# Optimization experiments

Hardware: AMD Instinct MI355X
Metric: run time of the kernel (lower is better)

Reference implementation:

```python
import jax, jax.numpy as jnp
import numpy as np

N = 50000
E = 800000
NODE_IN = 16
EDGE_IN = 8
HID = 128
OUT = 128
HEADS = 4
HC = HID // HEADS          # per-head channels = 32
EH = HID // 2              # edge hidden = 64
EPS = 1e-5
NEG_SLOPE = 0.2            # PyG GATConv leaky_relu slope


def setup_inputs() -> dict:
    key = jax.random.key(0)
    ks = list(jax.random.split(key, 16))
    it = iter(ks)
    nx = lambda: next(it)
    s = 0.05
    p = {}
    p["x"] = jax.random.normal(nx(), (N, NODE_IN), jnp.float32)
    p["edge_index"] = jax.random.randint(nx(), (2, E), 0, N)
    p["edge_attr"] = jax.random.normal(nx(), (E, EDGE_IN), jnp.float32)
    # node_preprocess: Linear + LayerNorm
    p["np_w"] = jax.random.normal(nx(), (NODE_IN, HID), jnp.float32) * s
    p["np_b"] = jnp.zeros((HID,), jnp.float32)
    p["np_g"] = jnp.ones((HID,), jnp.float32)
    p["np_be"] = jnp.zeros((HID,), jnp.float32)
    # edge_preprocess: Linear + LayerNorm
    p["ep_w"] = jax.random.normal(nx(), (EDGE_IN, EH), jnp.float32) * s
    p["ep_b"] = jnp.zeros((EH,), jnp.float32)
    p["ep_g"] = jnp.ones((EH,), jnp.float32)
    p["ep_be"] = jnp.zeros((EH,), jnp.float32)
    # 3 stacked GATConv layers (params stacked on leading dim)
    p["gat_w"] = jax.random.normal(nx(), (3, HID, HID), jnp.float32) * s
    p["gat_as"] = jax.random.normal(nx(), (3, HEADS, HC), jnp.float32) * s
    p["gat_ad"] = jax.random.normal(nx(), (3, HEADS, HC), jnp.float32) * s
    p["gat_ew"] = jax.random.normal(nx(), (3, EH, HID), jnp.float32) * s
    p["gat_ae"] = jax.random.normal(nx(), (3, HEADS, HC), jnp.float32) * s
    p["gat_b"] = jnp.zeros((3, HID), jnp.float32)
    # BatchNorm affine params
    p["bn_g"] = jnp.ones((3, HID), jnp.float32)
    p["bn_b"] = jnp.zeros((3, HID), jnp.float32)
    # final_proj: Linear + LayerNorm
    p["fp_w"] = jax.random.normal(nx(), (HID, OUT), jnp.float32) * s
    p["fp_b"] = jnp.zeros((OUT,), jnp.float32)
    p["fp_g"] = jnp.ones((OUT,), jnp.float32)
    p["fp_be"] = jnp.zeros((OUT,), jnp.float32)
    return p


def _ln(x, g, b):
    m = x.mean(-1, keepdims=True)
    v = ((x - m) ** 2).mean(-1, keepdims=True)
    return (x - m) * jax.lax.rsqrt(v + EPS) * g + b


def _bn(x, g, b):  # training-mode batch statistics over node dim
    m = x.mean(0)
    v = ((x - m) ** 2).mean(0)
    return (x - m) * jax.lax.rsqrt(v + EPS) * g + b


def _gat(h, e, src, dst, W, a_s, a_d, We, a_e, bias):
    # h: [N, HID], e: [E2, EH], src/dst: [E2]
    xs = (h @ W).reshape(N, HEADS, HC)                       # [N,H,C]
    al_s = (xs * a_s).sum(-1)                                # [N,H]
    al_d = (xs * a_d).sum(-1)                                # [N,H]
    eh = (e @ We).reshape(-1, HEADS, HC)                     # [E2,H,C]
    alpha = al_s[src] + al_d[dst] + (eh * a_e).sum(-1)       # [E2,H]
    alpha = jnp.where(alpha >= 0, alpha, NEG_SLOPE * alpha)  # leaky relu
    # segment softmax over incoming edges of each dst node
    amax = jax.ops.segment_max(alpha, dst, num_segments=N)
    ex = jnp.exp(alpha - amax[dst])
    w = ex / jax.ops.segment_sum(ex, dst, num_segments=N)[dst]
    msg = xs[src] * w[:, :, None]                            # [E2,H,C]
    out = jax.ops.segment_sum(msg, dst, num_segments=N)      # [N,H,C]
    return out.reshape(N, HID) + bias


def reference(x, edge_index, edge_attr, np_w, np_b, np_g, np_be,
              ep_w, ep_b, ep_g, ep_be,
              gat_w, gat_as, gat_ad, gat_ew, gat_ae, gat_b,
              bn_g, bn_b, fp_w, fp_b, fp_g, fp_be):
    src, dst = edge_index[0], edge_index[1]
    h = jax.nn.relu(_ln(x @ np_w + np_b, np_g, np_be))
    e = jax.nn.relu(_ln(edge_attr @ ep_w + ep_b, ep_g, ep_be))
    # PyG GATConv default add_self_loops=True, fill_value='mean':
    # self-loop edge_attr = mean of incoming edge_attr per dst node (0 if none)
    deg = jax.ops.segment_sum(jnp.ones((E,), e.dtype), dst, num_segments=N)
    loop_e = jax.ops.segment_sum(e, dst, num_segments=N) / jnp.maximum(deg, 1.0)[:, None]
    ar = jnp.arange(N)
    src2 = jnp.concatenate([src, ar])
    dst2 = jnp.concatenate([dst, ar])
    e2 = jnp.concatenate([e, loop_e], axis=0)
    for i in range(3):
        res = h
        h = _gat(h, e2, src2, dst2, gat_w[i], gat_as[i], gat_ad[i],
                 gat_ew[i], gat_ae[i], gat_b[i])
        h = jax.nn.relu(_bn(h, bn_g[i], bn_b[i]) + res)
    return _ln(h @ fp_w + fp_b, fp_g, fp_be)
```

## Files before the change

kernel.cpp:

```cpp
#include <hip/hip_runtime.h>
#include <hip/hip_bf16.h>
#include <math.h>

#define N_NODES 50000
#define N_EDGES 800000
#define EPS 1e-5f
#define SLOPE 0.2f

typedef unsigned int u32;
typedef unsigned short u16;
typedef float floatx4 __attribute__((ext_vector_type(4)));
typedef short short8_t __attribute__((ext_vector_type(8)));

__device__ __forceinline__ float bf2f(u16 v) {
    u32 u = ((u32)v) << 16;
    return __uint_as_float(u);
}
__device__ __forceinline__ u16 f2bf(float f) {
    u32 u = __float_as_uint(f);
    u32 r = (u + 0x7fffu + ((u >> 16) & 1u)) >> 16;
    return (u16)r;
}
__device__ __forceinline__ float lo_bf(u32 v) { return __uint_as_float(v << 16); }
__device__ __forceinline__ float hi_bf(u32 v) { return __uint_as_float(v & 0xffff0000u); }
__device__ __forceinline__ float wred(float v) {
    #pragma unroll
    for (int off = 32; off > 0; off >>= 1) v += __shfl_xor(v, off, 64);
    return v;
}

__global__ void k_M(const float* __restrict__ ew, const float* __restrict__ ae,
                    float* __restrict__ M) {
    int t = threadIdx.x;
    if (t >= 768) return;
    int k = t / 12, j = t % 12;
    int l = j >> 2, h = j & 3;
    const float* ewp = ew + l * 8192 + k * 128 + h * 32;
    const float* aep = ae + l * 128 + h * 32;
    float s = 0.f;
    #pragma unroll
    for (int c = 0; c < 32; c++) s += ewp[c] * aep[c];
    M[k * 12 + j] = s;
}

__global__ void k_convW(const float* __restrict__ w, u16* __restrict__ hi,
                        u16* __restrict__ lo, int total) {
    int i = blockIdx.x * 256 + threadIdx.x;
    if (i >= total) return;
    int l = i >> 14, r = i & 16383;
    int n = r >> 7, k = r & 127;
    float f = w[(size_t)l * 16384 + k * 128 + n];
    u16 hb = f2bf(f);
    hi[i] = hb;
    lo[i] = f2bf(f - bf2f(hb));
}

__global__ __launch_bounds__(256) void k_node_pre(
        const float* __restrict__ x, const float* __restrict__ w,
        const float* __restrict__ b, const float* __restrict__ g,
        const float* __restrict__ be, float* __restrict__ h) {
    int wave = threadIdx.x >> 6, lane = threadIdx.x & 63;
    int n = blockIdx.x * 4 + wave;
    if (n >= N_NODES) return;
    const float* xr = x + (size_t)n * 16;
    float xv[16];
    #pragma unroll
    for (int k = 0; k < 16; k++) xv[k] = xr[k];
    int c0 = lane, c1 = lane + 64;
    float a0 = b[c0], a1 = b[c1];
    #pragma unroll
    for (int k = 0; k < 16; k++) {
        a0 = fmaf(xv[k], w[k * 128 + c0], a0);
        a1 = fmaf(xv[k], w[k * 128 + c1], a1);
    }
    float m = wred(a0 + a1) * (1.f / 128.f);
    float d0 = a0 - m, d1 = a1 - m;
    float v = wred(d0 * d0 + d1 * d1) * (1.f / 128.f);
    float rs = rsqrtf(v + EPS);
    float o0 = d0 * rs * g[c0] + be[c0];
    float o1 = d1 * rs * g[c1] + be[c1];
    h[(size_t)n * 128 + c0] = fmaxf(o0, 0.f);
    h[(size_t)n * 128 + c1] = fmaxf(o1, 0.f);
}

__global__ void k_deg(const int* __restrict__ dst, int* __restrict__ deg,
                      int* __restrict__ rank) {
    int e = blockIdx.x * 256 + threadIdx.x;
    if (e < N_EDGES) rank[e] = atomicAdd(&deg[dst[e]], 1);
}

__global__ void k_scan1(const int* __restrict__ deg, int* __restrict__ incl,
                        int* __restrict__ bsum) {
    __shared__ int lds[1024];
    int i = blockIdx.x * 1024 + threadIdx.x;
    int v = (i < N_NODES) ? deg[i] : 0;
    lds[threadIdx.x] = v;
    __syncthreads();
    for (int off = 1; off < 1024; off <<= 1) {
        int t = (threadIdx.x >= off) ? lds[threadIdx.x - off] : 0;
        __syncthreads();
        lds[threadIdx.x] += t;
        __syncthreads();
    }
    if (i < N_NODES) incl[i] = lds[threadIdx.x];
    if (threadIdx.x == 1023) bsum[blockIdx.x] = lds[1023];
}
__global__ void k_scan2(int* __restrict__ bsum, int nb) {
    if (threadIdx.x == 0 && blockIdx.x == 0) {
        int run = 0;
        for (int i = 0; i < nb; i++) { int t = bsum[i]; bsum[i] = run; run += t; }
    }
}
__global__ void k_scan3(const int* __restrict__ incl, const int* __restrict__ bsum,
                        int* __restrict__ rowptr) {
    int i = blockIdx.x * 1024 + threadIdx.x;
    if (i < N_NODES) rowptr[i + 1] = incl[i] + bsum[blockIdx.x];
    if (i == 0) rowptr[0] = 0;
}

__global__ void k_fill(const int* __restrict__ ei, const int* __restrict__ rowptr,
                       const int* __restrict__ rank, int2* __restrict__ csr_se) {
    int e = blockIdx.x * 256 + threadIdx.x;
    if (e >= N_EDGES) return;
    int src = ei[e], dst = ei[N_EDGES + e];
    int slot = rowptr[dst] + rank[e];
    csr_se[slot] = make_int2(src, e);
}

__global__ __launch_bounds__(256) void k_edge_c(
        const int2* __restrict__ csr_se, const float* __restrict__ ea,
        const float* __restrict__ epw, const float* __restrict__ epb,
        const float* __restrict__ epg, const float* __restrict__ epbe,
        const float* __restrict__ M, int* __restrict__ csr_src,
        float* __restrict__ csr_aE) {
    __shared__ float sW[512], sM[768], sB[64], sG[64], sBe[64];
    for (int i = threadIdx.x; i < 512; i += 256) sW[i] = epw[i];
    for (int i = threadIdx.x; i < 768; i += 256) sM[i] = M[i];
    if (threadIdx.x < 64) {
        sB[threadIdx.x] = epb[threadIdx.x];
        sG[threadIdx.x] = epg[threadIdx.x];
        sBe[threadIdx.x] = epbe[threadIdx.x];
    }
    __syncthreads();
    int t = threadIdx.x;
    int s = blockIdx.x * 128 + (t >> 1);
    if (s >= N_EDGES) return;
    int hf = t & 1, cb = hf * 32;
    int2 se = csr_se[s];
    int src = se.x, e = se.y;
    float4 x0 = *(const float4*)(ea + (size_t)e * 8);
    float4 x1 = *(const float4*)(ea + (size_t)e * 8 + 4);
    float xa[8] = {x0.x, x0.y, x0.z, x0.w, x1.x, x1.y, x1.z, x1.w};
    float v[32];
    float sum = 0.f;
    #pragma unroll
    for (int c = 0; c < 32; c++) {
        float a = sB[cb + c];
        #pragma unroll
        for (int k = 0; k < 8; k++) a = fmaf(xa[k], sW[k * 64 + cb + c], a);
        v[c] = a; sum += a;
    }
    sum += __shfl_xor(sum, 1, 64);
    float m = sum * (1.f / 64.f);
    float var = 0.f;
    #pragma unroll
    for (int c = 0; c < 32; c++) { float d = v[c] - m; var += d * d; }
    var += __shfl_xor(var, 1, 64);
    float rs = rsqrtf(var * (1.f / 64.f) + EPS);
    #pragma unroll
    for (int c = 0; c < 32; c++) {
        float o = (v[c] - m) * rs * sG[cb + c] + sBe[cb + c];
        v[c] = fmaxf(o, 0.f);
    }
    float aE[12];
    #pragma unroll
    for (int j = 0; j < 12; j++) aE[j] = 0.f;
    #pragma unroll
    for (int c = 0; c < 32; c++) {
        float vc = v[c];
        #pragma unroll
        for (int j = 0; j < 12; j++) aE[j] = fmaf(vc, sM[(cb + c) * 12 + j], aE[j]);
    }
    #pragma unroll
    for (int j = 0; j < 12; j++) aE[j] += __shfl_xor(aE[j], 1, 64);
    if (hf == 0) {
        csr_src[s] = src;
        #pragma unroll
        for (int l = 0; l < 3; l++) {
            float4 w4;
            w4.x = aE[l * 4 + 0]; w4.y = aE[l * 4 + 1];
            w4.z = aE[l * 4 + 2]; w4.w = aE[l * 4 + 3];
            *(float4*)(csr_aE + ((size_t)l * N_EDGES + s) * 4) = w4;
        }
    }
}

__global__ __launch_bounds__(256) void k_gemm_xs_mfma(
        const float* __restrict__ h, const u16* __restrict__ wt_hi,
        const u16* __restrict__ wt_lo, u16* __restrict__ xs) {
    int wave = threadIdx.x >> 6, lane = threadIdx.x & 63;
    int r0 = (blockIdx.x * 4 + wave) * 16;
    if (r0 >= N_NODES) return;
    int lrow = lane & 15, lk = lane >> 4;
    const float* ap = h + (size_t)(r0 + lrow) * 128 + lk * 8;
    const u16* bph = wt_hi + lrow * 128 + lk * 8;
    const u16* bpl = wt_lo + lrow * 128 + lk * 8;
    floatx4 acc[8];
    #pragma unroll
    for (int j = 0; j < 8; j++) acc[j] = (floatx4){0.f, 0.f, 0.f, 0.f};
    #pragma unroll
    for (int s = 0; s < 4; s++) {
        float4 v0 = *(const float4*)(ap + s * 32);
        float4 v1 = *(const float4*)(ap + s * 32 + 4);
        float av[8] = {v0.x, v0.y, v0.z, v0.w, v1.x, v1.y, v1.z, v1.w};
        short8_t ahi, alo;
        #pragma unroll
        for (int i = 0; i < 8; i++) {
            u16 hb = f2bf(av[i]);
            ahi[i] = (short)hb;
            alo[i] = (short)f2bf(av[i] - bf2f(hb));
        }
        short8_t bh[8], bl[8];
        #pragma unroll
        for (int j = 0; j < 8; j++) {
            bh[j] = *(const short8_t*)(bph + s * 32 + j * 2048);
            bl[j] = *(const short8_t*)(bpl + s * 32 + j * 2048);
        }
        #pragma unroll
        for (int j = 0; j < 8; j++)
            acc[j] = __builtin_amdgcn_mfma_f32_16x16x32_bf16(ahi, bh[j], acc[j], 0, 0, 0);
        #pragma unroll
        for (int j = 0; j < 8; j++)
            acc[j] = __builtin_amdgcn_mfma_f32_16x16x32_bf16(ahi, bl[j], acc[j], 0, 0, 0);
        #pragma unroll
        for (int j = 0; j < 8; j++)
            acc[j] = __builtin_amdgcn_mfma_f32_16x16x32_bf16(alo, bh[j], acc[j], 0, 0, 0);
    }
    u16* orow = xs + (size_t)(r0 + lk * 4) * 128 + lrow;
    #pragma unroll
    for (int j = 0; j < 8; j++) {
        #pragma unroll
        for (int reg = 0; reg < 4; reg++)
            orow[(size_t)reg * 128 + j * 16] = f2bf(acc[j][reg]);
    }
}

__global__ void k_al(const u16* __restrict__ xs, const float* __restrict__ as_,
                     const float* __restrict__ ad_, float* __restrict__ al_s,
                     float* __restrict__ al_d) {
    int t = blockIdx.x * 256 + threadIdx.x;
    if (t >= N_NODES * 4) return;
    int n = t >> 2, hh = t & 3;
    const uint4* xp = (const uint4*)(xs + (size_t)n * 128 + hh * 32);
    const float* app = as_ + hh * 32;
    const float* dpp = ad_ + hh * 32;
    float s = 0.f, d = 0.f;
    #pragma unroll
    for (int q = 0; q < 4; q++) {
        uint4 v = xp[q];
        u32 wv[4] = {v.x, v.y, v.z, v.w};
        #pragma unroll
        for (int p = 0; p < 4; p++) {
            int c = q * 8 + p * 2;
            float fl = lo_bf(wv[p]), fh = hi_bf(wv[p]);
            s = fmaf(fl, app[c], s); s = fmaf(fh, app[c + 1], s);
            d = fmaf(fl, dpp[c], d); d = fmaf(fh, dpp[c + 1], d);
        }
    }
    al_s[t] = s; al_d[t] = d;
}

__global__ __launch_bounds__(256) void k_agg(
        const int* __restrict__ rowptr, const int* __restrict__ csr_src,
        const float* __restrict__ aEl, const float* __restrict__ al_s,
        const float* __restrict__ al_d, const u16* __restrict__ xs,
        const float* __restrict__ bias, float* __restrict__ outp) {
    int lane = threadIdx.x & 63;
    int n = __builtin_amdgcn_readfirstlane(blockIdx.x * 4 + (threadIdx.x >> 6));
    if (n >= N_NODES) return;
    int row = rowptr[n], end = rowptr[n + 1];
    int hh = lane >> 4;
    const u32* xsw = (const u32*)xs;
    float ald = al_d[n * 4 + hh];
    float asn = al_s[n * 4 + hh];
    u32 xnp = xsw[(size_t)n * 64 + lane];
    float acc0 = 0.f, acc1 = 0.f, ssum = 0.f, aes = 0.f;
    int slot = row;
    for (; slot + 8 <= end; slot += 8) {
        int sv[8]; float ae[8], asv[8]; u32 xv[8];
        #pragma unroll
        for (int i = 0; i < 8; i++) sv[i] = csr_src[slot + i];
        #pragma unroll
        for (int i = 0; i < 8; i++) ae[i] = aEl[(size_t)(slot + i) * 4 + hh];
        #pragma unroll
        for (int i = 0; i < 8; i++) asv[i] = al_s[sv[i] * 4 + hh];
        #pragma unroll
        for (int i = 0; i < 8; i++) xv[i] = xsw[(size_t)sv[i] * 64 + lane];
        #pragma unroll
        for (int i = 0; i < 8; i++) {
            aes += ae[i];
            float a = asv[i] + ald + ae[i]; a = (a >= 0.f) ? a : SLOPE * a;
            float ev = __expf(a);
            ssum += ev;
            acc0 = fmaf(ev, lo_bf(xv[i]), acc0);
            acc1 = fmaf(ev, hi_bf(xv[i]), acc1);
        }
    }
    for (; slot + 4 <= end; slot += 4) {
        int sv[4]; float ae[4], asv[4]; u32 xv[4];
        #pragma unroll
        for (int i = 0; i < 4; i++) sv[i] = csr_src[slot + i];
        #pragma unroll
        for (int i = 0; i < 4; i++) ae[i] = aEl[(size_t)(slot + i) * 4 + hh];
        #pragma unroll
        for (int i = 0; i < 4; i++) asv[i] = al_s[sv[i] * 4 + hh];
        #pragma unroll
        for (int i = 0; i < 4; i++) xv[i] = xsw[(size_t)sv[i] * 64 + lane];
        #pragma unroll
        for (int i = 0; i < 4; i++) {
            aes += ae[i];
            float a = asv[i] + ald + ae[i]; a = (a >= 0.f) ? a : SLOPE * a;
            float ev = __expf(a);
            ssum += ev;
            acc0 = fmaf(ev, lo_bf(xv[i]), acc0);
            acc1 = fmaf(ev, hi_bf(xv[i]), acc1);
        }
    }
    for (; slot < end; slot++) {
        int sA = csr_src[slot];
        float aeA = aEl[(size_t)slot * 4 + hh];
        float asA = al_s[sA * 4 + hh];
        u32 xA = xsw[(size_t)sA * 64 + lane];
        aes += aeA;
        float aA = asA + ald + aeA; aA = (aA >= 0.f) ? aA : SLOPE * aA;
        float eA = __expf(aA);
        ssum += eA;
        acc0 = fmaf(eA, lo_bf(xA), acc0); acc1 = fmaf(eA, hi_bf(xA), acc1);
    }
    float dinv = 1.f / fmaxf((float)(end - row), 1.f);
    float sa = asn + ald + aes * dinv; sa = (sa >= 0.f) ? sa : SLOPE * sa;
    float e = __expf(sa);
    ssum += e;
    acc0 = fmaf(e, lo_bf(xnp), acc0); acc1 = fmaf(e, hi_bf(xnp), acc1);
    float2 bv = *(const float2*)(bias + lane * 2);
    float2 o;
    o.x = acc0 / ssum + bv.x;
    o.y = acc1 / ssum + bv.y;
    *(float2*)(outp + (size_t)n * 128 + lane * 2) = o;
}

__global__ void k_bn_stats(const float* __restrict__ x, float* __restrict__ stats) {
    __shared__ float lds[512];
    int t = threadIdx.x;
    int c = t & 127, half = t >> 7;
    float s = 0.f, q = 0.f;
    for (int n = blockIdx.x * 2 + half; n < N_NODES; n += gridDim.x * 2) {
        float v = x[(size_t)n * 128 + c];
        s += v; q = fmaf(v, v, q);
    }
    lds[t] = s; lds[256 + t] = q;
    __syncthreads();
    if (t < 128) {
        atomicAdd(&stats[c], lds[t] + lds[t + 128]);
        atomicAdd(&stats[128 + c], lds[256 + t] + lds[256 + t + 128]);
    }
}

__global__ void k_bn_apply(const floatx4* __restrict__ outp, const float* __restrict__ stats,
                           const float* __restrict__ g, const float* __restrict__ b,
                           floatx4* __restrict__ h) {
    int idx = blockIdx.x * 256 + threadIdx.x;
    if (idx >= N_NODES * 32) return;
    int c0 = (idx & 31) * 4;
    floatx4 o = outp[idx], hv = h[idx], r;
    #pragma unroll
    for (int p = 0; p < 4; p++) {
        int c = c0 + p;
        float m = stats[c] * (1.f / N_NODES);
        float var = stats[128 + c] * (1.f / N_NODES) - m * m;
        float rs = rsqrtf(var + EPS);
        float v = (o[p] - m) * rs * g[c] + b[c] + hv[p];
        r[p] = fmaxf(v, 0.f);
    }
    h[idx] = r;
}

__global__ __launch_bounds__(256) void k_gemm_fp_mfma(
        const float* __restrict__ h, const u16* __restrict__ wt_hi,
        const u16* __restrict__ wt_lo, const float* __restrict__ fb,
        const float* __restrict__ g, const float* __restrict__ be,
        float* __restrict__ out) {
    int wave = threadIdx.x >> 6, lane = threadIdx.x & 63;
    int r0 = (blockIdx.x * 4 + wave) * 16;
    if (r0 >= N_NODES) return;
    int lrow = lane & 15, lk = lane >> 4;
    const float* ap = h + (size_t)(r0 + lrow) * 128 + lk * 8;
    const u16* bph = wt_hi + lrow * 128 + lk * 8;
    const u16* bpl = wt_lo + lrow * 128 + lk * 8;
    floatx4 acc[8];
    #pragma unroll
    for (int j = 0; j < 8; j++) acc[j] = (floatx4){0.f, 0.f, 0.f, 0.f};
    #pragma unroll
    for (int s = 0; s < 4; s++) {
        float4 v0 = *(const float4*)(ap + s * 32);
        float4 v1 = *(const float4*)(ap + s * 32 + 4);
        float av[8] = {v0.x, v0.y, v0.z, v0.w, v1.x, v1.y, v1.z, v1.w};
        short8_t ahi, alo;
        #pragma unroll
        for (int i = 0; i < 8; i++) {
            u16 hb = f2bf(av[i]);
            ahi[i] = (short)hb;
            alo[i] = (short)f2bf(av[i] - bf2f(hb));
        }
        short8_t bh[8], bl[8];
        #pragma unroll
        for (int j = 0; j < 8; j++) {
            bh[j] = *(const short8_t*)(bph + s * 32 + j * 2048);
            bl[j] = *(const short8_t*)(bpl + s * 32 + j * 2048);
        }
        #pragma unroll
        for (int j = 0; j < 8; j++)
            acc[j] = __builtin_amdgcn_mfma_f32_16x16x32_bf16(ahi, bh[j], acc[j], 0, 0, 0);
        #pragma unroll
        for (int j = 0; j < 8; j++)
            acc[j] = __builtin_amdgcn_mfma_f32_16x16x32_bf16(ahi, bl[j], acc[j], 0, 0, 0);
        #pragma unroll
        for (int j = 0; j < 8; j++)
            acc[j] = __builtin_amdgcn_mfma_f32_16x16x32_bf16(alo, bh[j], acc[j], 0, 0, 0);
    }
    float gv[8], bev[8];
    #pragma unroll
    for (int j = 0; j < 8; j++) {
        float fbv = fb[j * 16 + lrow];
        gv[j] = g[j * 16 + lrow];
        bev[j] = be[j * 16 + lrow];
        #pragma unroll
        for (int reg = 0; reg < 4; reg++) acc[j][reg] += fbv;
    }
    float s1[4] = {0.f, 0.f, 0.f, 0.f}, s2[4] = {0.f, 0.f, 0.f, 0.f};
    #pragma unroll
    for (int j = 0; j < 8; j++) {
        #pragma unroll
        for (int reg = 0; reg < 4; reg++) {
            float y = acc[j][reg];
            s1[reg] += y;
            s2[reg] = fmaf(y, y, s2[reg]);
        }
    }
    #pragma unroll
    for (int off = 1; off <= 8; off <<= 1) {
        #pragma unroll
        for (int reg = 0; reg < 4; reg++) {
            s1[reg] += __shfl_xor(s1[reg], off, 64);
            s2[reg] += __shfl_xor(s2[reg], off, 64);
        }
    }
    #pragma unroll
    for (int reg = 0; reg < 4; reg++) {
        float m = s1[reg] * (1.f / 128.f);
        float var = s2[reg] * (1.f / 128.f) - m * m;
        float rs = rsqrtf(var + EPS);
        float* orow = out + (size_t)(r0 + lk * 4 + reg) * 128 + lrow;
        #pragma unroll
        for (int j = 0; j < 8; j++)
            orow[j * 16] = (acc[j][reg] - m) * rs * gv[j] + bev[j];
    }
}

extern "C" void kernel_launch(void* const* d_in, const int* in_sizes, int n_in,
                              void* d_out, int out_size, void* d_ws, size_t ws_size,
                              hipStream_t stream) {
    const float* x      = (const float*)d_in[0];
    const int*   ei     = (const int*)d_in[1];
    const float* ea     = (const float*)d_in[2];
    const float* np_w   = (const float*)d_in[3];
    const float* np_b   = (const float*)d_in[4];
    const float* np_g   = (const float*)d_in[5];
    const float* np_be  = (const float*)d_in[6];
    const float* ep_w   = (const float*)d_in[7];
    const float* ep_b   = (const float*)d_in[8];
    const float* ep_g   = (const float*)d_in[9];
    const float* ep_be  = (const float*)d_in[10];
    const float* gat_w  = (const float*)d_in[11];
    const float* gat_as = (const float*)d_in[12];
    const float* gat_ad = (const float*)d_in[13];
    const float* gat_ew = (const float*)d_in[14];
    const float* gat_ae = (const float*)d_in[15];
    const float* gat_b  = (const float*)d_in[16];
    const float* bn_g   = (const float*)d_in[17];
    const float* bn_b   = (const float*)d_in[18];
    const float* fp_w   = (const float*)d_in[19];
    const float* fp_b   = (const float*)d_in[20];
    const float* fp_g   = (const float*)d_in[21];
    const float* fp_be  = (const float*)d_in[22];
    float* out = (float*)d_out;

    char* ws = (char*)d_ws;
    size_t off = 0;
    auto alloc = [&](size_t bytes) -> void* {
        void* p = ws + off;
        off = (off + bytes + 255) & ~(size_t)255;
        return p;
    };
    float* h      = (float*)alloc((size_t)N_NODES * 128 * 4);
    float* buf    = (float*)alloc((size_t)N_NODES * 128 * 4);
    u16*   xs     = (u16*)alloc((size_t)N_NODES * 128 * 2);
    float* al_s   = (float*)alloc((size_t)N_NODES * 4 * 4);
    float* al_d   = (float*)alloc((size_t)N_NODES * 4 * 4);
    int*   deg    = (int*)alloc((size_t)N_NODES * 4);
    int*   rowptr = (int*)alloc((size_t)(N_NODES + 1) * 4);
    int*   cursor = (int*)alloc((size_t)N_NODES * 4);
    int*   incl   = (int*)alloc((size_t)N_NODES * 4);
    int*   bsum   = (int*)alloc(64 * 4);
    int*   csr_src= (int*)alloc((size_t)N_EDGES * 4);
    float* csr_aE = (float*)alloc((size_t)N_EDGES * 12 * 4);
    float* M      = (float*)alloc(64 * 12 * 4);
    float* stats  = (float*)alloc(256 * 4);
    u16*   wt_hi  = (u16*)alloc((size_t)3 * 16384 * 2);
    u16*   wt_lo  = (u16*)alloc((size_t)3 * 16384 * 2);
    (void)cursor;
    int2*  csr_se = (int2*)buf;
    int*   rank   = (int*)xs;
    u16*   wtf_hi = (u16*)incl;
    u16*   wtf_lo = wtf_hi + 16384;

    hipMemsetAsync(deg, 0, (size_t)N_NODES * 4, stream);

    k_M<<<1, 768, 0, stream>>>(gat_ew, gat_ae, M);
    k_convW<<<192, 256, 0, stream>>>(gat_w, wt_hi, wt_lo, 3 * 16384);
    k_node_pre<<<(N_NODES + 3) / 4, 256, 0, stream>>>(x, np_w, np_b, np_g, np_be, h);
    k_deg<<<(N_EDGES + 255) / 256, 256, 0, stream>>>(ei + N_EDGES, deg, rank);
    int nblk = (N_NODES + 1023) / 1024;
    k_scan1<<<nblk, 1024, 0, stream>>>(deg, incl, bsum);
    k_scan2<<<1, 64, 0, stream>>>(bsum, nblk);
    k_scan3<<<nblk, 1024, 0, stream>>>(incl, bsum, rowptr);
    k_convW<<<64, 256, 0, stream>>>(fp_w, wtf_hi, wtf_lo, 16384);
    k_fill<<<(N_EDGES + 255) / 256, 256, 0, stream>>>(ei, rowptr, rank, csr_se);
    k_edge_c<<<(N_EDGES + 127) / 128, 256, 0, stream>>>(csr_se, ea, ep_w, ep_b, ep_g,
                                                        ep_be, M, csr_src, csr_aE);

    for (int l = 0; l < 3; l++) {
        k_gemm_xs_mfma<<<(3125 + 3) / 4, 256, 0, stream>>>(
            h, wt_hi + (size_t)l * 16384, wt_lo + (size_t)l * 16384, xs);
        k_al<<<(N_NODES * 4 + 255) / 256, 256, 0, stream>>>(xs, gat_as + l * 128,
                                                            gat_ad + l * 128, al_s, al_d);
        hipMemsetAsync(stats, 0, 256 * 4, stream);
        k_agg<<<(N_NODES + 3) / 4, 256, 0, stream>>>(rowptr, csr_src,
                                                     csr_aE + (size_t)l * N_EDGES * 4,
                                                     al_s, al_d, xs, gat_b + l * 128, buf);
        k_bn_stats<<<256, 256, 0, stream>>>(buf, stats);
        k_bn_apply<<<(N_NODES * 32 + 255) / 256, 256, 0, stream>>>(
            (const floatx4*)buf, stats, bn_g + l * 128, bn_b + l * 128, (floatx4*)h);
    }
    k_gemm_fp_mfma<<<(3125 + 3) / 4, 256, 0, stream>>>(
        h, wtf_hi, wtf_lo, fp_b, fp_g, fp_be, out);
}
```

Before: 699.2 us.

## Fuse BatchNorm apply into next GEMM and give edge preprocessing one thread per edge

Removes the separate BatchNorm-apply kernel. Normalisation, residual add and ReLU now run inside the next layer's GEMM prologue, which also writes the updated h back, and the last layer's BN is folded into the final projection GEMM. This saves one full read and write pass over the node features per layer plus three kernel launches. Separately, the edge preprocessing kernel now handles one edge per thread with vectorised floatx4 LDS math instead of splitting each edge across two lanes with shuffles, which raises per-thread register use.

```diff
diff --git a/kernel.cpp b/kernel.cpp
--- a/kernel.cpp
+++ b/kernel.cpp
@@ -133,76 +133,70 @@
         const float* __restrict__ epg, const float* __restrict__ epbe,
         const float* __restrict__ M, int* __restrict__ csr_src,
         float* __restrict__ csr_aE) {
-    __shared__ float sW[512], sM[768], sB[64], sG[64], sBe[64];
-    for (int i = threadIdx.x; i < 512; i += 256) sW[i] = epw[i];
-    for (int i = threadIdx.x; i < 768; i += 256) sM[i] = M[i];
-    if (threadIdx.x < 64) {
-        sB[threadIdx.x] = epb[threadIdx.x];
-        sG[threadIdx.x] = epg[threadIdx.x];
-        sBe[threadIdx.x] = epbe[threadIdx.x];
-    }
+    __shared__ floatx4 sW4[128], sM4[192], sB4[16], sG4[16], sBe4[16];
+    int tid = threadIdx.x;
+    if (tid < 128) sW4[tid] = ((const floatx4*)epw)[tid];
+    if (tid < 192) sM4[tid] = ((const floatx4*)M)[tid];
+    if (tid < 16) sB4[tid] = ((const floatx4*)epb)[tid];
+    if (tid >= 32 && tid < 48) sG4[tid - 32] = ((const floatx4*)epg)[tid - 32];
+    if (tid >= 64 && tid < 80) sBe4[tid - 64] = ((const floatx4*)epbe)[tid - 64];
     __syncthreads();
-    int t = threadIdx.x;
-    int s = blockIdx.x * 128 + (t >> 1);
+    int s = blockIdx.x * 256 + tid;
     if (s >= N_EDGES) return;
-    int hf = t & 1, cb = hf * 32;
     int2 se = csr_se[s];
     int src = se.x, e = se.y;
     float4 x0 = *(const float4*)(ea + (size_t)e * 8);
     float4 x1 = *(const float4*)(ea + (size_t)e * 8 + 4);
     float xa[8] = {x0.x, x0.y, x0.z, x0.w, x1.x, x1.y, x1.z, x1.w};
-    float v[32];
-    float sum = 0.f;
-    #pragma unroll
-    for (int c = 0; c < 32; c++) {
-        float a = sB[cb + c];
-        #pragma unroll
-        for (int k = 0; k < 8; k++) a = fmaf(xa[k], sW[k * 64 + cb + c], a);
-        v[c] = a; sum += a;
-    }
-    sum += __shfl_xor(sum, 1, 64);
-    float m = sum * (1.f / 64.f);
-    float var = 0.f;
-    #pragma unroll
-    for (int c = 0; c < 32; c++) { float d = v[c] - m; var += d * d; }
-    var += __shfl_xor(var, 1, 64);
-    float rs = rsqrtf(var * (1.f / 64.f) + EPS);
-    #pragma unroll
-    for (int c = 0; c < 32; c++) {
-        float o = (v[c] - m) * rs * sG[cb + c] + sBe[cb + c];
-        v[c] = fmaxf(o, 0.f);
-    }
-    float aE[12];
-    #pragma unroll
-    for (int j = 0; j < 12; j++) aE[j] = 0.f;
-    #pragma unroll
-    for (int c = 0; c < 32; c++) {
-        float vc = v[c];
-        #pragma unroll
-        for (int j = 0; j < 12; j++) aE[j] = fmaf(vc, sM[(cb + c) * 12 + j], aE[j]);
-    }
-    #pragma unroll
-    for (int j = 0; j < 12; j++) aE[j] += __shfl_xor(aE[j], 1, 64);
-    if (hf == 0) {
-        csr_src[s] = src;
-        #pragma unroll
-        for (int l = 0; l < 3; l++) {
-            float4 w4;
-            w4.x = aE[l * 4 + 0]; w4.y = aE[l * 4 + 1];
-            w4.z = aE[l * 4 + 2]; w4.w = aE[l * 4 + 3];
-            *(float4*)(csr_aE + ((size_t)l * N_EDGES + s) * 4) = w4;
-        }
-    }
+    floatx4 v4[16];
+    floatx4 sum4 = {0.f, 0.f, 0.f, 0.f};
+    #pragma unroll
+    for (int c4 = 0; c4 < 16; c4++) {
+        floatx4 a = sB4[c4];
+        #pragma unroll
+        for (int k = 0; k < 8; k++) a += xa[k] * sW4[k * 16 + c4];
+        v4[c4] = a;
+        sum4 += a;
+    }
+    float m = (sum4[0] + sum4[1] + sum4[2] + sum4[3]) * (1.f / 64.f);
+    floatx4 var4 = {0.f, 0.f, 0.f, 0.f};
+    #pragma unroll
+    for (int c4 = 0; c4 < 16; c4++) { floatx4 d = v4[c4] - m; var4 += d * d; }
+    float rs = rsqrtf((var4[0] + var4[1] + var4[2] + var4[3]) * (1.f / 64.f) + EPS);
+    #pragma unroll
+    for (int c4 = 0; c4 < 16; c4++) {
+        floatx4 o = (v4[c4] - m) * rs * sG4[c4] + sBe4[c4];
+        #pragma unroll
+        for (int p = 0; p < 4; p++) v4[c4][p] = fmaxf(o[p], 0.f);
+    }
+    floatx4 aE0 = {0.f, 0.f, 0.f, 0.f};
+    floatx4 aE1 = {0.f, 0.f, 0.f, 0.f};
+    floatx4 aE2 = {0.f, 0.f, 0.f, 0.f};
+    #pragma unroll
+    for (int c = 0; c < 64; c++) {
+        float vc = v4[c >> 2][c & 3];
+        aE0 += vc * sM4[c * 3 + 0];
+        aE1 += vc * sM4[c * 3 + 1];
+        aE2 += vc * sM4[c * 3 + 2];
+    }
+    csr_src[s] = src;
+    *(floatx4*)(csr_aE + ((size_t)0 * N_EDGES + s) * 4) = aE0;
+    *(floatx4*)(csr_aE + ((size_t)1 * N_EDGES + s) * 4) = aE1;
+    *(floatx4*)(csr_aE + ((size_t)2 * N_EDGES + s) * 4) = aE2;
 }
 
 __global__ __launch_bounds__(256) void k_gemm_xs_mfma(
-        const float* __restrict__ h, const u16* __restrict__ wt_hi,
-        const u16* __restrict__ wt_lo, u16* __restrict__ xs) {
+        float* __restrict__ h, const float* __restrict__ buf,
+        const float* __restrict__ stats, const float* __restrict__ bng,
+        const float* __restrict__ bnb, const u16* __restrict__ wt_hi,
+        const u16* __restrict__ wt_lo, u16* __restrict__ xs, int fuse) {
     int wave = threadIdx.x >> 6, lane = threadIdx.x & 63;
     int r0 = (blockIdx.x * 4 + wave) * 16;
     if (r0 >= N_NODES) return;
     int lrow = lane & 15, lk = lane >> 4;
-    const float* ap = h + (size_t)(r0 + lrow) * 128 + lk * 8;
+    size_t rowoff = (size_t)(r0 + lrow) * 128 + lk * 8;
+    float* hp = h + rowoff;
+    const float* bp = buf + rowoff;
     const u16* bph = wt_hi + lrow * 128 + lk * 8;
     const u16* bpl = wt_lo + lrow * 128 + lk * 8;
     floatx4 acc[8];
@@ -210,9 +204,32 @@
     for (int j = 0; j < 8; j++) acc[j] = (floatx4){0.f, 0.f, 0.f, 0.f};
     #pragma unroll
     for (int s = 0; s < 4; s++) {
-        float4 v0 = *(const float4*)(ap + s * 32);
-        float4 v1 = *(const float4*)(ap + s * 32 + 4);
-        float av[8] = {v0.x, v0.y, v0.z, v0.w, v1.x, v1.y, v1.z, v1.w};
+        float av[8];
+        float4 h0 = *(const float4*)(hp + s * 32);
+        float4 h1 = *(const float4*)(hp + s * 32 + 4);
+        float hv[8] = {h0.x, h0.y, h0.z, h0.w, h1.x, h1.y, h1.z, h1.w};
+        if (fuse) {
+            float4 b0 = *(const float4*)(bp + s * 32);
+            float4 b1 = *(const float4*)(bp + s * 32 + 4);
+            float bv[8] = {b0.x, b0.y, b0.z, b0.w, b1.x, b1.y, b1.z, b1.w};
+            #pragma unroll
+            for (int i = 0; i < 8; i++) {
+                int c = lk * 8 + s * 32 + i;
+                float m = stats[c] * (1.f / N_NODES);
+                float var = stats[128 + c] * (1.f / N_NODES) - m * m;
+                float rsn = rsqrtf(var + EPS);
+                float val = (bv[i] - m) * rsn * bng[c] + bnb[c] + hv[i];
+                av[i] = fmaxf(val, 0.f);
+            }
+            float4 w0, w1;
+            w0.x = av[0]; w0.y = av[1]; w0.z = av[2]; w0.w = av[3];
+            w1.x = av[4]; w1.y = av[5]; w1.z = av[6]; w1.w = av[7];
+            *(float4*)(hp + s * 32) = w0;
+            *(float4*)(hp + s * 32 + 4) = w1;
+        } else {
+            #pragma unroll
+            for (int i = 0; i < 8; i++) av[i] = hv[i];
+        }
         short8_t ahi, alo;
         #pragma unroll
         for (int i = 0; i < 8; i++) {
@@ -366,27 +383,10 @@
     }
 }
 
-__global__ void k_bn_apply(const floatx4* __restrict__ outp, const float* __restrict__ stats,
-                           const float* __restrict__ g, const float* __restrict__ b,
-                           floatx4* __restrict__ h) {
-    int idx = blockIdx.x * 256 + threadIdx.x;
-    if (idx >= N_NODES * 32) return;
-    int c0 = (idx & 31) * 4;
-    floatx4 o = outp[idx], hv = h[idx], r;
-    #pragma unroll
-    for (int p = 0; p < 4; p++) {
-        int c = c0 + p;
-        float m = stats[c] * (1.f / N_NODES);
-        float var = stats[128 + c] * (1.f / N_NODES) - m * m;
-        float rs = rsqrtf(var + EPS);
-        float v = (o[p] - m) * rs * g[c] + b[c] + hv[p];
-        r[p] = fmaxf(v, 0.f);
-    }
-    h[idx] = r;
-}
-
 __global__ __launch_bounds__(256) void k_gemm_fp_mfma(
-        const float* __restrict__ h, const u16* __restrict__ wt_hi,
+        const float* __restrict__ h, const float* __restrict__ buf,
+        const float* __restrict__ stats, const float* __restrict__ bng,
+        const float* __restrict__ bnb, const u16* __restrict__ wt_hi,
         const u16* __restrict__ wt_lo, const float* __restrict__ fb,
         const float* __restrict__ g, const float* __restrict__ be,
         float* __restrict__ out) {
@@ -394,7 +394,9 @@
     int r0 = (blockIdx.x * 4 + wave) * 16;
     if (r0 >= N_NODES) return;
     int lrow = lane & 15, lk = lane >> 4;
-    const float* ap = h + (size_t)(r0 + lrow) * 128 + lk * 8;
+    size_t rowoff = (size_t)(r0 + lrow) * 128 + lk * 8;
+    const float* hp = h + rowoff;
+    const float* bp = buf + rowoff;
     const u16* bph = wt_hi + lrow * 128 + lk * 8;
     const u16* bpl = wt_lo + lrow * 128 + lk * 8;
     floatx4 acc[8];
@@ -402,9 +404,22 @@
     for (int j = 0; j < 8; j++) acc[j] = (floatx4){0.f, 0.f, 0.f, 0.f};
     #pragma unroll
     for (int s = 0; s < 4; s++) {
-        float4 v0 = *(const float4*)(ap + s * 32);
-        float4 v1 = *(const float4*)(ap + s * 32 + 4);
-        float av[8] = {v0.x, v0.y, v0.z, v0.w, v1.x, v1.y, v1.z, v1.w};
+        float4 h0 = *(const float4*)(hp + s * 32);
+        float4 h1 = *(const float4*)(hp + s * 32 + 4);
+        float4 b0 = *(const float4*)(bp + s * 32);
+        float4 b1 = *(const float4*)(bp + s * 32 + 4);
+        float hv[8] = {h0.x, h0.y, h0.z, h0.w, h1.x, h1.y, h1.z, h1.w};
+        float bvv[8] = {b0.x, b0.y, b0.z, b0.w, b1.x, b1.y, b1.z, b1.w};
+        float av[8];
+        #pragma unroll
+        for (int i = 0; i < 8; i++) {
+            int c = lk * 8 + s * 32 + i;
+            float m = stats[c] * (1.f / N_NODES);
+            float var = stats[128 + c] * (1.f / N_NODES) - m * m;
+            float rsn = rsqrtf(var + EPS);
+            float val = (bvv[i] - m) * rsn * bng[c] + bnb[c] + hv[i];
+            av[i] = fmaxf(val, 0.f);
+        }
         short8_t ahi, alo;
         #pragma unroll
         for (int i = 0; i < 8; i++) {
@@ -536,12 +551,14 @@
     k_scan3<<<nblk, 1024, 0, stream>>>(incl, bsum, rowptr);
     k_convW<<<64, 256, 0, stream>>>(fp_w, wtf_hi, wtf_lo, 16384);
     k_fill<<<(N_EDGES + 255) / 256, 256, 0, stream>>>(ei, rowptr, rank, csr_se);
-    k_edge_c<<<(N_EDGES + 127) / 128, 256, 0, stream>>>(csr_se, ea, ep_w, ep_b, ep_g,
+    k_edge_c<<<(N_EDGES + 255) / 256, 256, 0, stream>>>(csr_se, ea, ep_w, ep_b, ep_g,
                                                         ep_be, M, csr_src, csr_aE);
 
     for (int l = 0; l < 3; l++) {
         k_gemm_xs_mfma<<<(3125 + 3) / 4, 256, 0, stream>>>(
-            h, wt_hi + (size_t)l * 16384, wt_lo + (size_t)l * 16384, xs);
+            h, buf, stats, bn_g + (l > 0 ? (l - 1) * 128 : 0),
+            bn_b + (l > 0 ? (l - 1) * 128 : 0),
+            wt_hi + (size_t)l * 16384, wt_lo + (size_t)l * 16384, xs, l > 0 ? 1 : 0);
         k_al<<<(N_NODES * 4 + 255) / 256, 256, 0, stream>>>(xs, gat_as + l * 128,
                                                             gat_ad + l * 128, al_s, al_d);
         hipMemsetAsync(stats, 0, 256 * 4, stream);
@@ -549,9 +566,8 @@
                                                      csr_aE + (size_t)l * N_EDGES * 4,
                                                      al_s, al_d, xs, gat_b + l * 128, buf);
         k_bn_stats<<<256, 256, 0, stream>>>(buf, stats);
-        k_bn_apply<<<(N_NODES * 32 + 255) / 256, 256, 0, stream>>>(
-            (const floatx4*)buf, stats, bn_g + l * 128, bn_b + l * 128, (floatx4*)h);
     }
     k_gemm_fp_mfma<<<(3125 + 3) / 4, 256, 0, stream>>>(
-        h, wtf_hi, wtf_lo, fp_b, fp_g, fp_be, out);
-}
+        h, buf, stats, bn_g + 2 * 128, bn_b + 2 * 128,
+        wtf_hi, wtf_lo, fp_b, fp_g, fp_be, out);
+}
```

Result: faster. 672.0 us (median of 2 runs) (-3.9%).
